# Kernel tuning notes

Hardware: AMD Instinct MI355X
Metric: run time of the kernel (lower is better)

## Reference

```python
import jax, jax.numpy as jnp
import numpy as np

N_NODES = 50000
N_EDGES = 800000
C_IN, C_HID, C_OUT = 256, 128, 64


def gcn_conv(x, src, dst, deg_inv_sqrt, W, b, n_nodes):
    """PyG GCNConv with self-loops already folded into (src, dst, deg).

    out[j] = sum_{(i->j)} d_i^{-1/2} d_j^{-1/2} (x W)[i] + b
    """
    h = x @ W  # [N, out]
    norm = deg_inv_sqrt[src] * deg_inv_sqrt[dst]  # [E+N]
    msg = h[src] * norm[:, None]  # [E+N, out]
    out = jax.ops.segment_sum(msg, dst, num_segments=n_nodes)
    return out + b


def setup_inputs() -> dict:
    key = jax.random.key(0)
    k1, k2, k3, k4, k5, k6 = jax.random.split(key, 6)
    x = jax.random.normal(k1, (N_NODES, C_IN), dtype=jnp.float32)
    edge_index = jax.random.randint(k2, (2, N_EDGES), 0, N_NODES, dtype=jnp.int64)
    # Glorot-ish init for GCN weights
    W1 = jax.random.normal(k3, (C_IN, C_HID), dtype=jnp.float32) / np.sqrt(C_IN)
    b1 = jnp.zeros((C_HID,), dtype=jnp.float32)
    W2 = jax.random.normal(k4, (C_HID, C_OUT), dtype=jnp.float32) / np.sqrt(C_HID)
    b2 = jnp.zeros((C_OUT,), dtype=jnp.float32)
    return {"x": x, "edge_index": edge_index, "W1": W1, "b1": b1, "W2": W2, "b2": b2}


def reference(x, edge_index, W1, b1, W2, b2):
    n = x.shape[0]
    loop = jnp.arange(n, dtype=edge_index.dtype)
    src = jnp.concatenate([edge_index[0], loop])  # row (message source)
    dst = jnp.concatenate([edge_index[1], loop])  # col (aggregation target)
    # symmetric normalization degree: in-degree at dst, with self loops
    deg = jax.ops.segment_sum(jnp.ones_like(dst, dtype=x.dtype), dst, num_segments=n)
    deg_inv_sqrt = jnp.where(deg > 0, jax.lax.rsqrt(deg), 0.0)

    h = gcn_conv(x, src, dst, deg_inv_sqrt, W1, b1, n)
    h = jax.nn.relu(h)
    # Dropout is identity in eval mode (reference baseline is deterministic)
    out = gcn_conv(h, src, dst, deg_inv_sqrt, W2, b2, n)
    return out
```

## Files before the change

kernel.cpp:

```cpp
#include <hip/hip_runtime.h>


#define CIN 256
#define CHID 128
#define COUT 64
#define NSCAT 256

typedef unsigned short ushort_t;
typedef unsigned int uint_t;
typedef __attribute__((ext_vector_type(8))) short short8;
typedef __attribute__((ext_vector_type(4))) float f32x4;

__device__ inline ushort_t f2bf(float f) {
  union { float f; uint_t u; } v; v.f = f;
  uint_t r = v.u + 0x7FFFu + ((v.u >> 16) & 1u);
  return (ushort_t)(r >> 16);
}
__device__ inline float bf2f(ushort_t u) {
  union { uint_t u; float f; } v; v.u = ((uint_t)u) << 16;
  return v.f;
}
__device__ inline float bf_lo(uint_t u) {
  union { uint_t u; float f; } v; v.u = u << 16;
  return v.f;
}
__device__ inline float bf_hi(uint_t u) {
  union { uint_t u; float f; } v; v.u = u & 0xFFFF0000u;
  return v.f;
}
__device__ inline uint_t pack2(float a, float b) {
  return (uint_t)f2bf(a) | ((uint_t)f2bf(b) << 16);
}

__global__ void k_wt2(const float* __restrict__ W1, const float* __restrict__ W2,
                      ushort_t* __restrict__ Wt1, ushort_t* __restrict__ Wt2) {
  int i = blockIdx.x * blockDim.x + threadIdx.x;
  if (i < CIN * CHID) {
    int k = i % CIN, c = i / CIN;
    Wt1[i] = f2bf(W1[(size_t)k * CHID + c]);
  } else {
    int j = i - CIN * CHID;
    if (j < CHID * COUT) {
      int k = j % CHID, c = j / CHID;
      Wt2[j] = f2bf(W2[(size_t)k * COUT + c]);
    }
  }
}


__global__ __launch_bounds__(256) void k_bhist(const int* __restrict__ dst,
                                               int* __restrict__ cntmat,
                                               int e, int nbk) {
  __shared__ int h[256];
  const int tid = threadIdx.x;
  h[tid] = 0;
  __syncthreads();
  const int per = (e + gridDim.x - 1) / gridDim.x;
  const int lo = blockIdx.x * per;
  const int hi = min(e, lo + per);
  for (int i = lo + tid; i < hi; i += 256) atomicAdd(&h[dst[i] >> 8], 1);
  __syncthreads();
  if (tid < nbk) cntmat[blockIdx.x * nbk + tid] = h[tid];
}

__global__ __launch_bounds__(256) void k_colscan(int* __restrict__ cntmat,
                                                 int* __restrict__ btot, int nbk) {
  __shared__ int s[NSCAT];
  const int k = blockIdx.x;
  const int tid = threadIdx.x;
  const int v = cntmat[tid * nbk + k];
  s[tid] = v;
  __syncthreads();
  for (int off = 1; off < NSCAT; off <<= 1) {
    int t = (tid >= off) ? s[tid - off] : 0;
    __syncthreads();
    s[tid] += t;
    __syncthreads();
  }
  cntmat[tid * nbk + k] = s[tid] - v;
  if (tid == NSCAT - 1) btot[k] = s[tid];
}

__global__ __launch_bounds__(256) void k_btscan(const int* __restrict__ btot,
                                                int* __restrict__ bbase,
                                                int nbk, int e) {
  __shared__ int s[256];
  const int tid = threadIdx.x;
  const int v = (tid < nbk) ? btot[tid] : 0;
  s[tid] = v;
  __syncthreads();
  for (int off = 1; off < 256; off <<= 1) {
    int t = (tid >= off) ? s[tid - off] : 0;
    __syncthreads();
    s[tid] += t;
    __syncthreads();
  }
  if (tid < nbk) bbase[tid] = s[tid] - v;
  if (tid == 0) bbase[nbk] = e;
}

__global__ __launch_bounds__(256) void k_bscatter(const int* __restrict__ src,
                                                  const int* __restrict__ dst,
                                                  const int* __restrict__ cntmat,
                                                  const int* __restrict__ bbase,
                                                  int2* __restrict__ pairs,
                                                  int e, int nbk) {
  __shared__ int cur[256];
  const int tid = threadIdx.x;
  cur[tid] = (tid < nbk) ? (bbase[tid] + cntmat[blockIdx.x * nbk + tid]) : 0;
  __syncthreads();
  const int per = (e + gridDim.x - 1) / gridDim.x;
  const int lo = blockIdx.x * per;
  const int hi = min(e, lo + per);
  for (int i = lo + tid; i < hi; i += 256) {
    int d = dst[i];
    int off = atomicAdd(&cur[d >> 8], 1);
    int2 p;
    p.x = d;
    p.y = src[i];
    pairs[off] = p;
  }
}

__global__ __launch_bounds__(256) void k_bbuild(const int2* __restrict__ pairs,
                                                const int* __restrict__ bbase,
                                                int* __restrict__ rowptr,
                                                float* __restrict__ dinv,
                                                int* __restrict__ csr, int n, int e) {
  __shared__ int h[256];
  __shared__ int s[256];
  const int tid = threadIdx.x;
  const int b = blockIdx.x;
  const int lo = bbase[b];
  const int hi = bbase[b + 1];
  h[tid] = 0;
  __syncthreads();
  for (int i = lo + tid; i < hi; i += 256) atomicAdd(&h[pairs[i].x & 255], 1);
  __syncthreads();
  const int deg = h[tid];
  s[tid] = deg;
  __syncthreads();
  for (int off = 1; off < 256; off <<= 1) {
    int t = (tid >= off) ? s[tid - off] : 0;
    __syncthreads();
    s[tid] += t;
    __syncthreads();
  }
  const int excl = s[tid] - deg;
  const int node = (b << 8) + tid;
  if (node < n) {
    rowptr[node] = lo + excl;
    dinv[node] = rsqrtf((float)(deg + 1));
  }
  if (b == 0 && tid == 0) rowptr[n] = e;
  h[tid] = lo + excl;
  __syncthreads();
  for (int i = lo + tid; i < hi; i += 256) {
    int2 p = pairs[i];
    int slot = atomicAdd(&h[p.x & 255], 1);
    csr[slot] = p.y;
  }
}

template <int K, int BN, bool XBF16>
__global__ __launch_bounds__(256) void k_gemm_mfma(
    const void* __restrict__ Xv, const ushort_t* __restrict__ Wt,
    const float* __restrict__ dinv, ushort_t* __restrict__ out, int M) {
  constexpr int BM = 128, BK = 32;
  constexpr int NSUB = BN / 16;
  constexpr int ASZ = BM * BK;
  constexpr int BSZ = BK * BN;
  constexpr int NCH = K / BK;
  constexpr int AIT = ASZ / 8 / 256;
  constexpr int BIT = BSZ / 8 / 256;

  __shared__ ushort_t As[2][ASZ];
  __shared__ ushort_t Bs[2][BSZ];

  const int tid = threadIdx.x;
  const int lane = tid & 63;
  const int w = tid >> 6;
  const int row0 = blockIdx.x * BM;

  const float* Xf = (const float*)Xv;
  const ushort_t* Xb = (const ushort_t*)Xv;

  float4 ar0[AIT], ar1[AIT];
  uint4 arb[AIT];
  uint4 brg[BIT];

  auto load_A = [&](int kc) {
#pragma unroll
    for (int i = 0; i < AIT; ++i) {
      int fi = i * 256 + tid;
      int r = fi & 127, k0 = (fi >> 7) * 8;
      int gr = row0 + r;
      if (gr > M - 1) gr = M - 1;
      if (XBF16) {
        arb[i] = *(const uint4*)(Xb + (size_t)gr * K + kc + k0);
      } else {
        ar0[i] = *(const float4*)(Xf + (size_t)gr * K + kc + k0);
        ar1[i] = *(const float4*)(Xf + (size_t)gr * K + kc + k0 + 4);
      }
    }
#pragma unroll
    for (int i = 0; i < BIT; ++i) {
      int g = i * 256 + tid;
      int nf = g >> 6, l = g & 63;
      int c = nf * 16 + (l & 15), k0 = (l >> 4) * 8;
      brg[i] = *(const uint4*)(Wt + (size_t)c * K + kc + k0);
    }
  };

  auto write_lds = [&](int buf) {
#pragma unroll
    for (int i = 0; i < AIT; ++i) {
      int fi = i * 256 + tid;
      int r = fi & 127, kb = fi >> 7;
      int flat = (r >> 4) * 512 + ((r & 15) + 16 * kb) * 8;
      if (XBF16) {
        *(uint4*)&As[buf][flat] = arb[i];
      } else {
        uint4 p;
        p.x = pack2(ar0[i].x, ar0[i].y);
        p.y = pack2(ar0[i].z, ar0[i].w);
        p.z = pack2(ar1[i].x, ar1[i].y);
        p.w = pack2(ar1[i].z, ar1[i].w);
        *(uint4*)&As[buf][flat] = p;
      }
    }
#pragma unroll
    for (int i = 0; i < BIT; ++i) {
      int g = i * 256 + tid;
      int nf = g >> 6, l = g & 63;
      *(uint4*)&Bs[buf][nf * 512 + l * 8] = brg[i];
    }
  };

  f32x4 acc[2][NSUB];
#pragma unroll
  for (int mi = 0; mi < 2; ++mi)
#pragma unroll
    for (int ni = 0; ni < NSUB; ++ni)
      acc[mi][ni] = (f32x4){0.f, 0.f, 0.f, 0.f};

  load_A(0);
  write_lds(0);

#pragma unroll 1
  for (int ch = 0; ch < NCH; ++ch) {
    const int cur = ch & 1;
    __syncthreads();
    if (ch + 1 < NCH) load_A((ch + 1) * BK);

    short8 af[2];
#pragma unroll
    for (int mi = 0; mi < 2; ++mi)
      af[mi] = *(const short8*)&As[cur][(2 * w + mi) * 512 + lane * 8];
    short8 bf[NSUB];
#pragma unroll
    for (int ni = 0; ni < NSUB; ++ni)
      bf[ni] = *(const short8*)&Bs[cur][ni * 512 + lane * 8];

#pragma unroll
    for (int mi = 0; mi < 2; ++mi)
#pragma unroll
      for (int ni = 0; ni < NSUB; ++ni)
        acc[mi][ni] = __builtin_amdgcn_mfma_f32_16x16x32_bf16(
            af[mi], bf[ni], acc[mi][ni], 0, 0, 0);

    if (ch + 1 < NCH) write_lds(cur ^ 1);
  }

  const int qrow = (lane >> 4) * 4;
  const int col16 = lane & 15;
#pragma unroll
  for (int mi = 0; mi < 2; ++mi) {
    int rbase = row0 + w * 32 + mi * 16 + qrow;
#pragma unroll
    for (int v = 0; v < 4; ++v) {
      int row = rbase + v;
      if (row < M) {
        float dn = dinv[row];
#pragma unroll
        for (int ni = 0; ni < NSUB; ++ni)
          out[(size_t)row * BN + ni * 16 + col16] = f2bf(dn * acc[mi][ni][v]);
      }
    }
  }
}

__global__ __launch_bounds__(256) void k_aggw_h(
    const ushort_t* __restrict__ hh, const int* __restrict__ rowptr,
    const int* __restrict__ csr, const float* __restrict__ dinv,
    const float* __restrict__ bias, ushort_t* __restrict__ out, int n) {
  const int tid = threadIdx.x;
  const int node = blockIdx.x * 4 + (tid >> 6);
  if (node >= n) return;
  const int lane = tid & 63;
  const int q = lane & 15;
  const int eg = lane >> 4;

  float acc[8];
#pragma unroll
  for (int j = 0; j < 8; ++j) acc[j] = 0.0f;

  const int beg = rowptr[node];
  const int end = rowptr[node + 1];
  for (int k = beg + eg; k < end; k += 4) {
    int s = csr[k];
    uint4 u = *(const uint4*)&hh[(size_t)s * CHID + q * 8];
    acc[0] += bf_lo(u.x); acc[1] += bf_hi(u.x);
    acc[2] += bf_lo(u.y); acc[3] += bf_hi(u.y);
    acc[4] += bf_lo(u.z); acc[5] += bf_hi(u.z);
    acc[6] += bf_lo(u.w); acc[7] += bf_hi(u.w);
  }
#pragma unroll
  for (int j = 0; j < 8; ++j) {
    acc[j] += __shfl_xor(acc[j], 16);
    acc[j] += __shfl_xor(acc[j], 32);
  }
  if (eg == 0) {
    uint4 u = *(const uint4*)&hh[(size_t)node * CHID + q * 8];
    acc[0] += bf_lo(u.x); acc[1] += bf_hi(u.x);
    acc[2] += bf_lo(u.y); acc[3] += bf_hi(u.y);
    acc[4] += bf_lo(u.z); acc[5] += bf_hi(u.z);
    acc[6] += bf_lo(u.w); acc[7] += bf_hi(u.w);
    const float dn = dinv[node];
    float4 b0 = *(const float4*)&bias[q * 8];
    float4 b1 = *(const float4*)&bias[q * 8 + 4];
    float r[8];
    r[0] = dn * acc[0] + b0.x; r[1] = dn * acc[1] + b0.y;
    r[2] = dn * acc[2] + b0.z; r[3] = dn * acc[3] + b0.w;
    r[4] = dn * acc[4] + b1.x; r[5] = dn * acc[5] + b1.y;
    r[6] = dn * acc[6] + b1.z; r[7] = dn * acc[7] + b1.w;
#pragma unroll
    for (int j = 0; j < 8; ++j) r[j] = fmaxf(r[j], 0.0f);
    uint4 o;
    o.x = pack2(r[0], r[1]); o.y = pack2(r[2], r[3]);
    o.z = pack2(r[4], r[5]); o.w = pack2(r[6], r[7]);
    *(uint4*)&out[(size_t)node * CHID + q * 8] = o;
  }
}

__global__ __launch_bounds__(256) void k_aggw_o(
    const ushort_t* __restrict__ hh, const int* __restrict__ rowptr,
    const int* __restrict__ csr, const float* __restrict__ dinv,
    const float* __restrict__ bias, float* __restrict__ out, int n) {
  const int tid = threadIdx.x;
  const int node = blockIdx.x * 4 + (tid >> 6);
  if (node >= n) return;
  const int lane = tid & 63;
  const int q = lane & 7;
  const int eg = lane >> 3;

  float acc[8];
#pragma unroll
  for (int j = 0; j < 8; ++j) acc[j] = 0.0f;

  const int beg = rowptr[node];
  const int end = rowptr[node + 1];
  for (int k = beg + eg; k < end; k += 8) {
    int s = csr[k];
    uint4 u = *(const uint4*)&hh[(size_t)s * COUT + q * 8];
    acc[0] += bf_lo(u.x); acc[1] += bf_hi(u.x);
    acc[2] += bf_lo(u.y); acc[3] += bf_hi(u.y);
    acc[4] += bf_lo(u.z); acc[5] += bf_hi(u.z);
    acc[6] += bf_lo(u.w); acc[7] += bf_hi(u.w);
  }
#pragma unroll
  for (int j = 0; j < 8; ++j) {
    acc[j] += __shfl_xor(acc[j], 8);
    acc[j] += __shfl_xor(acc[j], 16);
    acc[j] += __shfl_xor(acc[j], 32);
  }
  if (eg == 0) {
    uint4 u = *(const uint4*)&hh[(size_t)node * COUT + q * 8];
    acc[0] += bf_lo(u.x); acc[1] += bf_hi(u.x);
    acc[2] += bf_lo(u.y); acc[3] += bf_hi(u.y);
    acc[4] += bf_lo(u.z); acc[5] += bf_hi(u.z);
    acc[6] += bf_lo(u.w); acc[7] += bf_hi(u.w);
    const float dn = dinv[node];
    float4 b0 = *(const float4*)&bias[q * 8];
    float4 b1 = *(const float4*)&bias[q * 8 + 4];
    float4 o0, o1;
    o0.x = dn * acc[0] + b0.x; o0.y = dn * acc[1] + b0.y;
    o0.z = dn * acc[2] + b0.z; o0.w = dn * acc[3] + b0.w;
    o1.x = dn * acc[4] + b1.x; o1.y = dn * acc[5] + b1.y;
    o1.z = dn * acc[6] + b1.z; o1.w = dn * acc[7] + b1.w;
    *(float4*)&out[(size_t)node * COUT + q * 8] = o0;
    *(float4*)&out[(size_t)node * COUT + q * 8 + 4] = o1;
  }
}

extern "C" void kernel_launch(void* const* d_in, const int* in_sizes, int n_in,
                              void* d_out, int out_size, void* d_ws, size_t ws_size,
                              hipStream_t stream) {
  const float* x  = (const float*)d_in[0];
  const int*   ei = (const int*)d_in[1];
  const float* W1 = (const float*)d_in[2];
  const float* b1 = (const float*)d_in[3];
  const float* W2 = (const float*)d_in[4];
  const float* b2 = (const float*)d_in[5];
  float* out = (float*)d_out;

  const int n = in_sizes[0] / CIN;
  const int e = in_sizes[1] / 2;
  const int* src = ei;
  const int* dst = ei + e;
  const int nbk = (n + 255) >> 8;

  size_t off = 0;
  auto alloc = [&](size_t bytes) {
    size_t o = off;
    off = (off + bytes + 255) & ~(size_t)255;
    return o;
  };
  char* ws = (char*)d_ws;
  int*      cntmat = (int*)(ws + alloc((size_t)NSCAT * 256 * 4));
  int*      btot   = (int*)(ws + alloc(256 * 4));
  int*      bbase  = (int*)(ws + alloc(257 * 4));
  int*      rowptr = (int*)(ws + alloc((size_t)(n + 1) * 4));
  float*    dinv   = (float*)(ws + alloc((size_t)n * 4));
  int*      csr    = (int*)(ws + alloc((size_t)e * 4));
  int2*     pairs  = (int2*)(ws + alloc((size_t)e * 8));
  ushort_t* wt1    = (ushort_t*)(ws + alloc((size_t)CIN * CHID * 2));
  ushort_t* wt2    = (ushort_t*)(ws + alloc((size_t)CHID * COUT * 2));
  ushort_t* hhA    = (ushort_t*)(ws + alloc((size_t)n * CHID * 2));
  ushort_t* hhB    = (ushort_t*)(ws + alloc((size_t)n * CHID * 2));

  k_wt2<<<(CIN * CHID + CHID * COUT + 255) / 256, 256, 0, stream>>>(W1, W2, wt1, wt2);

  k_bhist<<<NSCAT, 256, 0, stream>>>(dst, cntmat, e, nbk);
  k_colscan<<<nbk, NSCAT, 0, stream>>>(cntmat, btot, nbk);
  k_btscan<<<1, 256, 0, stream>>>(btot, bbase, nbk, e);
  k_bscatter<<<NSCAT, 256, 0, stream>>>(src, dst, cntmat, bbase, pairs, e, nbk);
  k_bbuild<<<nbk, 256, 0, stream>>>(pairs, bbase, rowptr, dinv, csr, n, e);

  k_gemm_mfma<CIN, CHID, false><<<(n + 127) / 128, 256, 0, stream>>>(
      x, wt1, dinv, hhA, n);
  k_aggw_h<<<(n + 3) / 4, 256, 0, stream>>>(hhA, rowptr, csr, dinv, b1, hhB, n);

  k_gemm_mfma<CHID, COUT, true><<<(n + 127) / 128, 256, 0, stream>>>(
      hhB, wt2, dinv, hhA, n);
  k_aggw_o<<<(n + 3) / 4, 256, 0, stream>>>(hhA, rowptr, csr, dinv, b2, out, n);
}
```

Before: 139.3 us.

## Compact edge pairs and CSR indices, fuse prep kernels, shrink GEMM row tile

Merges the weight conversion into the histogram kernel and removes the separate bucket-base scan kernel by recomputing the small scan inside the scatter and build kernels. Edge pairs are packed into one 32-bit word and CSR source indices are stored as 16-bit, halving index traffic in the build and both aggregation passes. The GEMM row tile drops from 128 to 64 for more blocks. The 16-bit indices limit correctness to graphs with at most 65536 nodes, and the scan is now repeated redundantly in every block.

```diff
diff --git a/kernel.cpp b/kernel.cpp
--- a/kernel.cpp
+++ b/kernel.cpp
@@ -16,10 +16,6 @@
   uint_t r = v.u + 0x7FFFu + ((v.u >> 16) & 1u);
   return (ushort_t)(r >> 16);
 }
-__device__ inline float bf2f(ushort_t u) {
-  union { uint_t u; float f; } v; v.u = ((uint_t)u) << 16;
-  return v.f;
-}
 __device__ inline float bf_lo(uint_t u) {
   union { uint_t u; float f; } v; v.u = u << 16;
   return v.f;
@@ -32,35 +28,37 @@
   return (uint_t)f2bf(a) | ((uint_t)f2bf(b) << 16);
 }
 
-__global__ void k_wt2(const float* __restrict__ W1, const float* __restrict__ W2,
-                      ushort_t* __restrict__ Wt1, ushort_t* __restrict__ Wt2) {
-  int i = blockIdx.x * blockDim.x + threadIdx.x;
-  if (i < CIN * CHID) {
-    int k = i % CIN, c = i / CIN;
-    Wt1[i] = f2bf(W1[(size_t)k * CHID + c]);
+__global__ __launch_bounds__(256) void k_pre(const int* __restrict__ dst,
+                                             int* __restrict__ cntmat,
+                                             const float* __restrict__ W1,
+                                             const float* __restrict__ W2,
+                                             ushort_t* __restrict__ Wt1,
+                                             ushort_t* __restrict__ Wt2,
+                                             int e, int nbk) {
+  const int tid = threadIdx.x;
+  if (blockIdx.x < NSCAT) {
+    __shared__ int h[256];
+    h[tid] = 0;
+    __syncthreads();
+    const int per = (e + NSCAT - 1) / NSCAT;
+    const int lo = blockIdx.x * per;
+    const int hi = min(e, lo + per);
+    for (int i = lo + tid; i < hi; i += 256) atomicAdd(&h[dst[i] >> 8], 1);
+    __syncthreads();
+    if (tid < nbk) cntmat[blockIdx.x * nbk + tid] = h[tid];
   } else {
-    int j = i - CIN * CHID;
-    if (j < CHID * COUT) {
-      int k = j % CHID, c = j / CHID;
-      Wt2[j] = f2bf(W2[(size_t)k * COUT + c]);
-    }
-  }
-}
-
-
-__global__ __launch_bounds__(256) void k_bhist(const int* __restrict__ dst,
-                                               int* __restrict__ cntmat,
-                                               int e, int nbk) {
-  __shared__ int h[256];
-  const int tid = threadIdx.x;
-  h[tid] = 0;
-  __syncthreads();
-  const int per = (e + gridDim.x - 1) / gridDim.x;
-  const int lo = blockIdx.x * per;
-  const int hi = min(e, lo + per);
-  for (int i = lo + tid; i < hi; i += 256) atomicAdd(&h[dst[i] >> 8], 1);
-  __syncthreads();
-  if (tid < nbk) cntmat[blockIdx.x * nbk + tid] = h[tid];
+    int i = (blockIdx.x - NSCAT) * 256 + tid;
+    if (i < CIN * CHID) {
+      int k = i % CIN, c = i / CIN;
+      Wt1[i] = f2bf(W1[(size_t)k * CHID + c]);
+    } else {
+      int j = i - CIN * CHID;
+      if (j < CHID * COUT) {
+        int k = j % CHID, c = j / CHID;
+        Wt2[j] = f2bf(W2[(size_t)k * COUT + c]);
+      }
+    }
+  }
 }
 
 __global__ __launch_bounds__(256) void k_colscan(int* __restrict__ cntmat,
@@ -81,61 +79,68 @@
   if (tid == NSCAT - 1) btot[k] = s[tid];
 }
 
-__global__ __launch_bounds__(256) void k_btscan(const int* __restrict__ btot,
-                                                int* __restrict__ bbase,
-                                                int nbk, int e) {
-  __shared__ int s[256];
-  const int tid = threadIdx.x;
-  const int v = (tid < nbk) ? btot[tid] : 0;
-  s[tid] = v;
-  __syncthreads();
-  for (int off = 1; off < 256; off <<= 1) {
-    int t = (tid >= off) ? s[tid - off] : 0;
-    __syncthreads();
-    s[tid] += t;
-    __syncthreads();
-  }
-  if (tid < nbk) bbase[tid] = s[tid] - v;
-  if (tid == 0) bbase[nbk] = e;
-}
-
 __global__ __launch_bounds__(256) void k_bscatter(const int* __restrict__ src,
                                                   const int* __restrict__ dst,
                                                   const int* __restrict__ cntmat,
-                                                  const int* __restrict__ bbase,
-                                                  int2* __restrict__ pairs,
+                                                  const int* __restrict__ btot,
+                                                  int* __restrict__ pairs,
                                                   int e, int nbk) {
+  __shared__ int s[256];
   __shared__ int cur[256];
   const int tid = threadIdx.x;
-  cur[tid] = (tid < nbk) ? (bbase[tid] + cntmat[blockIdx.x * nbk + tid]) : 0;
-  __syncthreads();
-  const int per = (e + gridDim.x - 1) / gridDim.x;
+  const int v = (tid < nbk) ? btot[tid] : 0;
+  s[tid] = v;
+  __syncthreads();
+  for (int off = 1; off < 256; off <<= 1) {
+    int t = (tid >= off) ? s[tid - off] : 0;
+    __syncthreads();
+    s[tid] += t;
+    __syncthreads();
+  }
+  cur[tid] = (tid < nbk) ? (s[tid] - v + cntmat[blockIdx.x * nbk + tid]) : 0;
+  __syncthreads();
+  const int per = (e + NSCAT - 1) / NSCAT;
   const int lo = blockIdx.x * per;
   const int hi = min(e, lo + per);
   for (int i = lo + tid; i < hi; i += 256) {
     int d = dst[i];
     int off = atomicAdd(&cur[d >> 8], 1);
-    int2 p;
-    p.x = d;
-    p.y = src[i];
-    pairs[off] = p;
-  }
-}
-
-__global__ __launch_bounds__(256) void k_bbuild(const int2* __restrict__ pairs,
-                                                const int* __restrict__ bbase,
+    pairs[off] = (src[i] << 8) | (d & 255);
+  }
+}
+
+__global__ __launch_bounds__(256) void k_bbuild(const int* __restrict__ pairs,
+                                                const int* __restrict__ btot,
                                                 int* __restrict__ rowptr,
                                                 float* __restrict__ dinv,
-                                                int* __restrict__ csr, int n, int e) {
+                                                ushort_t* __restrict__ csr,
+                                                int n, int e, int nbk) {
   __shared__ int h[256];
   __shared__ int s[256];
+  __shared__ int sbnd[2];
   const int tid = threadIdx.x;
   const int b = blockIdx.x;
-  const int lo = bbase[b];
-  const int hi = bbase[b + 1];
+  {
+    const int v = (tid < nbk) ? btot[tid] : 0;
+    s[tid] = v;
+    __syncthreads();
+    for (int off = 1; off < 256; off <<= 1) {
+      int t = (tid >= off) ? s[tid - off] : 0;
+      __syncthreads();
+      s[tid] += t;
+      __syncthreads();
+    }
+    if (tid == b) {
+      sbnd[0] = s[tid] - v;
+      sbnd[1] = s[tid];
+    }
+    __syncthreads();
+  }
+  const int lo = sbnd[0];
+  const int hi = sbnd[1];
   h[tid] = 0;
   __syncthreads();
-  for (int i = lo + tid; i < hi; i += 256) atomicAdd(&h[pairs[i].x & 255], 1);
+  for (int i = lo + tid; i < hi; i += 256) atomicAdd(&h[pairs[i] & 255], 1);
   __syncthreads();
   const int deg = h[tid];
   s[tid] = deg;
@@ -156,17 +161,18 @@
   h[tid] = lo + excl;
   __syncthreads();
   for (int i = lo + tid; i < hi; i += 256) {
-    int2 p = pairs[i];
-    int slot = atomicAdd(&h[p.x & 255], 1);
-    csr[slot] = p.y;
-  }
-}
-
-template <int K, int BN, bool XBF16>
+    int p = pairs[i];
+    int slot = atomicAdd(&h[p & 255], 1);
+    csr[slot] = (ushort_t)(((uint_t)p) >> 8);
+  }
+}
+
+template <int K, int BN, int BM, bool XBF16>
 __global__ __launch_bounds__(256) void k_gemm_mfma(
     const void* __restrict__ Xv, const ushort_t* __restrict__ Wt,
     const float* __restrict__ dinv, ushort_t* __restrict__ out, int M) {
-  constexpr int BM = 128, BK = 32;
+  constexpr int BK = 32;
+  constexpr int MI = BM / 64;
   constexpr int NSUB = BN / 16;
   constexpr int ASZ = BM * BK;
   constexpr int BSZ = BK * BN;
@@ -193,7 +199,7 @@
 #pragma unroll
     for (int i = 0; i < AIT; ++i) {
       int fi = i * 256 + tid;
-      int r = fi & 127, k0 = (fi >> 7) * 8;
+      int r = fi % BM, k0 = (fi / BM) * 8;
       int gr = row0 + r;
       if (gr > M - 1) gr = M - 1;
       if (XBF16) {
@@ -216,7 +222,7 @@
 #pragma unroll
     for (int i = 0; i < AIT; ++i) {
       int fi = i * 256 + tid;
-      int r = fi & 127, kb = fi >> 7;
+      int r = fi % BM, kb = fi / BM;
       int flat = (r >> 4) * 512 + ((r & 15) + 16 * kb) * 8;
       if (XBF16) {
         *(uint4*)&As[buf][flat] = arb[i];
@@ -237,9 +243,9 @@
     }
   };
 
-  f32x4 acc[2][NSUB];
-#pragma unroll
-  for (int mi = 0; mi < 2; ++mi)
+  f32x4 acc[MI][NSUB];
+#pragma unroll
+  for (int mi = 0; mi < MI; ++mi)
 #pragma unroll
     for (int ni = 0; ni < NSUB; ++ni)
       acc[mi][ni] = (f32x4){0.f, 0.f, 0.f, 0.f};
@@ -253,17 +259,17 @@
     __syncthreads();
     if (ch + 1 < NCH) load_A((ch + 1) * BK);
 
-    short8 af[2];
-#pragma unroll
-    for (int mi = 0; mi < 2; ++mi)
-      af[mi] = *(const short8*)&As[cur][(2 * w + mi) * 512 + lane * 8];
+    short8 af[MI];
+#pragma unroll
+    for (int mi = 0; mi < MI; ++mi)
+      af[mi] = *(const short8*)&As[cur][(w * MI + mi) * 512 + lane * 8];
     short8 bf[NSUB];
 #pragma unroll
     for (int ni = 0; ni < NSUB; ++ni)
       bf[ni] = *(const short8*)&Bs[cur][ni * 512 + lane * 8];
 
 #pragma unroll
-    for (int mi = 0; mi < 2; ++mi)
+    for (int mi = 0; mi < MI; ++mi)
 #pragma unroll
       for (int ni = 0; ni < NSUB; ++ni)
         acc[mi][ni] = __builtin_amdgcn_mfma_f32_16x16x32_bf16(
@@ -275,8 +281,8 @@
   const int qrow = (lane >> 4) * 4;
   const int col16 = lane & 15;
 #pragma unroll
-  for (int mi = 0; mi < 2; ++mi) {
-    int rbase = row0 + w * 32 + mi * 16 + qrow;
+  for (int mi = 0; mi < MI; ++mi) {
+    int rbase = row0 + (w * MI + mi) * 16 + qrow;
 #pragma unroll
     for (int v = 0; v < 4; ++v) {
       int row = rbase + v;
@@ -292,7 +298,7 @@
 
 __global__ __launch_bounds__(256) void k_aggw_h(
     const ushort_t* __restrict__ hh, const int* __restrict__ rowptr,
-    const int* __restrict__ csr, const float* __restrict__ dinv,
+    const ushort_t* __restrict__ csr, const float* __restrict__ dinv,
     const float* __restrict__ bias, ushort_t* __restrict__ out, int n) {
   const int tid = threadIdx.x;
   const int node = blockIdx.x * 4 + (tid >> 6);
@@ -345,7 +351,7 @@
 
 __global__ __launch_bounds__(256) void k_aggw_o(
     const ushort_t* __restrict__ hh, const int* __restrict__ rowptr,
-    const int* __restrict__ csr, const float* __restrict__ dinv,
+    const ushort_t* __restrict__ csr, const float* __restrict__ dinv,
     const float* __restrict__ bias, float* __restrict__ out, int n) {
   const int tid = threadIdx.x;
   const int node = blockIdx.x * 4 + (tid >> 6);
@@ -419,29 +425,27 @@
   char* ws = (char*)d_ws;
   int*      cntmat = (int*)(ws + alloc((size_t)NSCAT * 256 * 4));
   int*      btot   = (int*)(ws + alloc(256 * 4));
-  int*      bbase  = (int*)(ws + alloc(257 * 4));
   int*      rowptr = (int*)(ws + alloc((size_t)(n + 1) * 4));
   float*    dinv   = (float*)(ws + alloc((size_t)n * 4));
-  int*      csr    = (int*)(ws + alloc((size_t)e * 4));
-  int2*     pairs  = (int2*)(ws + alloc((size_t)e * 8));
+  ushort_t* csr    = (ushort_t*)(ws + alloc((size_t)e * 2));
+  int*      pairs  = (int*)(ws + alloc((size_t)e * 4));
   ushort_t* wt1    = (ushort_t*)(ws + alloc((size_t)CIN * CHID * 2));
   ushort_t* wt2    = (ushort_t*)(ws + alloc((size_t)CHID * COUT * 2));
   ushort_t* hhA    = (ushort_t*)(ws + alloc((size_t)n * CHID * 2));
   ushort_t* hhB    = (ushort_t*)(ws + alloc((size_t)n * CHID * 2));
 
-  k_wt2<<<(CIN * CHID + CHID * COUT + 255) / 256, 256, 0, stream>>>(W1, W2, wt1, wt2);
-
-  k_bhist<<<NSCAT, 256, 0, stream>>>(dst, cntmat, e, nbk);
+  const int WTB = (CIN * CHID + CHID * COUT + 255) / 256;
+
+  k_pre<<<NSCAT + WTB, 256, 0, stream>>>(dst, cntmat, W1, W2, wt1, wt2, e, nbk);
   k_colscan<<<nbk, NSCAT, 0, stream>>>(cntmat, btot, nbk);
-  k_btscan<<<1, 256, 0, stream>>>(btot, bbase, nbk, e);
-  k_bscatter<<<NSCAT, 256, 0, stream>>>(src, dst, cntmat, bbase, pairs, e, nbk);
-  k_bbuild<<<nbk, 256, 0, stream>>>(pairs, bbase, rowptr, dinv, csr, n, e);
-
-  k_gemm_mfma<CIN, CHID, false><<<(n + 127) / 128, 256, 0, stream>>>(
+  k_bscatter<<<NSCAT, 256, 0, stream>>>(src, dst, cntmat, btot, pairs, e, nbk);
+  k_bbuild<<<nbk, 256, 0, stream>>>(pairs, btot, rowptr, dinv, csr, n, e, nbk);
+
+  k_gemm_mfma<CIN, CHID, 64, false><<<(n + 63) / 64, 256, 0, stream>>>(
       x, wt1, dinv, hhA, n);
   k_aggw_h<<<(n + 3) / 4, 256, 0, stream>>>(hhA, rowptr, csr, dinv, b1, hhB, n);
 
-  k_gemm_mfma<CHID, COUT, true><<<(n + 127) / 128, 256, 0, stream>>>(
+  k_gemm_mfma<CHID, COUT, 64, true><<<(n + 63) / 64, 256, 0, stream>>>(
       hhB, wt2, dinv, hhA, n);
   k_aggw_o<<<(n + 3) / 4, 256, 0, stream>>>(hhA, rowptr, csr, dinv, b2, out, n);
 }
```

Measured after the change: 139.6 us. No clear change (+0.2%).
